# Kernel optimization log

Measured on AMD Instinct MI355X. Metric: run time of the kernel, lower is better.

Reference implementation:

```python
import jax, jax.numpy as jnp
import numpy as np

# model constants (match init_kwargs)
D_EQUI = 64
D_INV = 256
D_INV_COND = 256
D_MSG = 64
N_HEADS = 16
D_FF = 256
D_EDGE_IN = 64
D_EDGE_OUT = 64
D_OUT = D_EQUI + N_HEADS + D_EDGE_OUT  # 144
IN_FEATS = 2 * D_MSG + D_EQUI + D_EDGE_IN  # 256
NEG = -1e9

B, N, NC = 2, 256, 512


def setup_inputs() -> dict:
    key = jax.random.key(0)
    ks = jax.random.split(key, 20)
    s = 0.02
    inp = {
        'equis': jax.random.normal(ks[0], (B, N, 3, D_EQUI), jnp.float32),
        'invs': jax.random.normal(ks[1], (B, N, D_INV), jnp.float32),
        'cond_equis': jax.random.normal(ks[2], (B, NC, 3, D_EQUI), jnp.float32),
        'cond_invs': jax.random.normal(ks[3], (B, NC, D_INV_COND), jnp.float32),
        'edges': jax.random.normal(ks[4], (B, N, NC, D_EDGE_IN), jnp.float32),
        'adj_matrix': jax.random.randint(ks[5], (B, N, NC), 0, 2, jnp.int32),
        # pairwise message params
        'q_w': s * jax.random.normal(ks[6], (D_INV, D_MSG), jnp.float32),
        'q_b': jnp.zeros((D_MSG,), jnp.float32),
        'k_w': s * jax.random.normal(ks[7], (D_INV_COND, D_MSG), jnp.float32),
        'k_b': jnp.zeros((D_MSG,), jnp.float32),
        'w1': s * jax.random.normal(ks[8], (IN_FEATS, D_FF), jnp.float32),
        'b1': jnp.zeros((D_FF,), jnp.float32),
        'w2': s * jax.random.normal(ks[9], (D_FF, D_OUT), jnp.float32),
        'b2': jnp.zeros((D_OUT,), jnp.float32),
        # equi attention params (bias-free linears)
        'equi_in_w': s * jax.random.normal(ks[10], (D_EQUI, D_EQUI), jnp.float32),
        'equi_out_w': s * jax.random.normal(ks[11], (D_EQUI, D_EQUI), jnp.float32),
        # inv attention params
        'inv_in_w': s * jax.random.normal(ks[12], (D_INV_COND, D_INV_COND), jnp.float32),
        'inv_in_b': jnp.zeros((D_INV_COND,), jnp.float32),
        'inv_out_w': s * jax.random.normal(ks[13], (D_INV_COND, D_INV), jnp.float32),
        'inv_out_b': jnp.zeros((D_INV,), jnp.float32),
    }
    return inp


def reference(equis, invs, cond_equis, cond_invs, edges, adj_matrix,
              q_w, q_b, k_w, k_b, w1, b1, w2, b2,
              equi_in_w, equi_out_w, inv_in_w, inv_in_b, inv_out_w, inv_out_b):
    # adjacency -> additive attention mask [B,N,NC]
    mask = jnp.where(adj_matrix > 0, 0.0, NEG).astype(equis.dtype)

    # ---- pairwise messages ----
    # per-channel dot products over the coordinate axis: [B,N,NC,D_EQUI]
    dot = jnp.einsum('bqxd,bkxd->bqkd', equis, cond_equis)
    q_msg = invs @ q_w + q_b            # [B,N,D_MSG]
    k_msg = cond_invs @ k_w + k_b       # [B,NC,D_MSG]
    feats = jnp.concatenate([
        jnp.broadcast_to(q_msg[:, :, None, :], (B, N, NC, D_MSG)),
        jnp.broadcast_to(k_msg[:, None, :, :], (B, N, NC, D_MSG)),
        dot,
        edges,
    ], axis=-1)                          # [B,N,NC,IN_FEATS]
    h = jax.nn.silu(feats @ w1 + b1)
    messages = h @ w2 + b2               # [B,N,NC,D_OUT]

    equi_m = messages[..., :D_EQUI]
    inv_m = messages[..., D_EQUI:D_EQUI + N_HEADS]
    edge_out = messages[..., D_EQUI + N_HEADS:]

    # ---- equivariant attention ----
    proj = jnp.einsum('bkxd,de->bkxe', cond_equis, equi_in_w)  # [B,NC,3,D_EQUI]
    attn_e = jax.nn.softmax(equi_m + mask[..., None], axis=2)   # [B,N,NC,D_EQUI]
    eo = jnp.einsum('bqkd,bkxd->bqxd', attn_e, proj)            # [B,N,3,D_EQUI]
    w_e = jnp.sqrt(jnp.sum(attn_e ** 2, axis=2))                # [B,N,D_EQUI]
    eo = eo * w_e[:, :, None, :]
    equi_out = jnp.einsum('bqxd,de->bqxe', eo, equi_out_w)

    # ---- invariant attention ----
    pf = cond_invs @ inv_in_w + inv_in_b                        # [B,NC,D_INV_COND]
    hf = pf.reshape(B, NC, N_HEADS, D_INV_COND // N_HEADS)      # [B,NC,H,dh]
    attn_i = jax.nn.softmax(inv_m + mask[..., None], axis=2)    # [B,N,NC,H]
    io = jnp.einsum('bqkh,bkhd->bqhd', attn_i, hf)              # [B,N,H,dh]
    w_i = jnp.sqrt(jnp.sum(attn_i ** 2, axis=2))                # [B,N,H]
    io = (io * w_i[..., None]).reshape(B, N, D_INV_COND)
    inv_out = io @ inv_out_w + inv_out_b                        # [B,N,D_INV]

    return equi_out, inv_out, edge_out
```

## Files before the change

kernel.cpp:

```cpp
#include <hip/hip_runtime.h>
#include <hip/hip_bf16.h>

#define DEVINL static __device__ __forceinline__

typedef __attribute__((ext_vector_type(8))) short bf16x8;
typedef __attribute__((ext_vector_type(8))) unsigned short us8;
typedef __attribute__((ext_vector_type(4))) float f32x4;
typedef __attribute__((ext_vector_type(4))) unsigned short us4;

DEVINL float siluf(float x) { return x / (1.0f + __expf(-x)); }
DEVINL unsigned short bfb(float x) { __hip_bfloat16 h = __float2bfloat16(x); return *(unsigned short*)&h; }
DEVINL float b2f(unsigned short u) { return __uint_as_float(((unsigned int)u) << 16); }

__global__ void wfrag_kernel(const float* __restrict__ w1, const float* __restrict__ w2,
                             unsigned short* __restrict__ w1f, unsigned short* __restrict__ w2f) {
  const int g = blockIdx.x, tid = threadIdx.x;
  if (g < 16) {
    #pragma unroll
    for (int e2 = 0; e2 < 16; ++e2) {
      const int flat = tid * 16 + e2;
      const int kk = flat >> 9, rem = flat & 511, ln = rem >> 3, e = rem & 7;
      const int c = g * 16 + (ln & 15);
      const int k = kk * 32 + (ln >> 4) * 8 + e;
      w1f[(size_t)g * 4096 + flat] = bfb(w1[(size_t)k * 256 + c]);
    }
  } else {
    const int t = g - 16;
    #pragma unroll
    for (int e2 = 0; e2 < 16; ++e2) {
      const int flat = tid * 16 + e2;
      const int kk = flat >> 9, rem = flat & 511, ln = rem >> 3, e = rem & 7;
      const int c = t * 16 + (ln & 15);
      const int k = kk * 32 + (ln >> 4) * 8 + e;
      w2f[(size_t)t * 4096 + flat] = bfb(w2[(size_t)k * 144 + c]);
    }
  }
}

__global__ void qk_kernel(const float* __restrict__ invs, const float* __restrict__ cond_invs,
                          const float* __restrict__ qw, const float* __restrict__ qb,
                          const float* __restrict__ kw, const float* __restrict__ kb2,
                          float* __restrict__ qm, float* __restrict__ km) {
  __shared__ float srow[256];
  const int r = blockIdx.x;
  const float* in; const float* w; const float* bias; float* out; int row;
  if (r < 512) { in = invs;      w = qw; bias = qb;  out = qm; row = r; }
  else         { in = cond_invs; w = kw; bias = kb2; out = km; row = r - 512; }
  for (int k = threadIdx.x; k < 256; k += 64) srow[k] = in[(size_t)row * 256 + k];
  __syncthreads();
  const int c = threadIdx.x;
  float acc = bias[c];
  for (int k = 0; k < 256; ++k) acc += srow[k] * w[(size_t)k * 64 + c];
  out[(size_t)row * 64 + c] = acc;
}

__global__ void projt_kernel(const float* __restrict__ ce, const float* __restrict__ eiw,
                             float* __restrict__ projt) {
  __shared__ float srow[64];
  const int r = blockIdx.x;
  const int b = r / 1536, rr = r % 1536, kn = rr / 3, x = rr % 3;
  srow[threadIdx.x] = ce[(size_t)r * 64 + threadIdx.x];
  __syncthreads();
  const int c = threadIdx.x;
  float acc = 0.f;
  for (int k = 0; k < 64; ++k) acc += srow[k] * eiw[(size_t)k * 64 + c];
  projt[((size_t)(b * 3 + x) * 64 + c) * 512 + kn] = acc;
}

__global__ void pft_kernel(const float* __restrict__ ci, const float* __restrict__ iiw,
                           const float* __restrict__ iib, float* __restrict__ pft) {
  __shared__ float srow[256];
  const int r = blockIdx.x, b = r >> 9, kn = r & 511;
  srow[threadIdx.x] = ci[(size_t)r * 256 + threadIdx.x];
  __syncthreads();
  const int c = threadIdx.x;
  float acc = iib[c];
  for (int k = 0; k < 256; ++k) acc += srow[k] * iiw[(size_t)k * 256 + c];
  pft[((size_t)(b * 256) + c) * 512 + kn] = acc;
}

__global__ __launch_bounds__(256, 2) void msg_kernel(
    const float* __restrict__ equis, const float* __restrict__ cond_equis,
    const float* __restrict__ edges,
    const float* __restrict__ qm, const float* __restrict__ km,
    const unsigned short* __restrict__ w1f, const float* __restrict__ b1,
    const unsigned short* __restrict__ w2f, const float* __restrict__ b2,
    float* __restrict__ edge_out, __hip_bfloat16* __restrict__ sct) {
  __shared__ __align__(16) unsigned short buf[64][264];
  __shared__ float eq_s[192];
  unsigned short (*score_s)[92] = (unsigned short (*)[92])&buf[0][0];
  float (*edge_s)[68]           = (float (*)[68])((char*)&buf[0][0] + 11776);

  const int bq = blockIdx.x >> 3;
  const int b  = bq >> 8;
  const int k0 = (blockIdx.x & 7) * 64;
  const int tid = threadIdx.x;
  const int lane = tid & 63, wn = tid >> 6;
  const int lj  = lane & 15;
  const int lkb = (lane >> 4) * 8;
  const int lr4 = (lane >> 4) * 4;

  if (tid < 192) eq_s[tid] = equis[(size_t)bq * 192 + tid];

  bf16x8 qf[2];
  {
    const float* qmr = qm + (size_t)bq * 64;
    #pragma unroll
    for (int kk = 0; kk < 2; ++kk) {
      const float4 a = *(const float4*)&qmr[kk * 32 + (lane >> 4) * 8];
      const float4 c = *(const float4*)&qmr[kk * 32 + (lane >> 4) * 8 + 4];
      bf16x8 v;
      v[0] = (short)bfb(a.x); v[1] = (short)bfb(a.y); v[2] = (short)bfb(a.z); v[3] = (short)bfb(a.w);
      v[4] = (short)bfb(c.x); v[5] = (short)bfb(c.y); v[6] = (short)bfb(c.z); v[7] = (short)bfb(c.w);
      qf[kk] = v;
    }
  }
  __syncthreads();

  #pragma unroll
  for (int it = 0; it < 4; ++it) {
    const int flat = it * 256 + tid, row = flat >> 4, seg = flat & 15;
    const float4 v = *(const float4*)&km[((size_t)(b * 512 + k0 + row)) * 64 + seg * 4];
    us4 u = { bfb(v.x), bfb(v.y), bfb(v.z), bfb(v.w) };
    *(us4*)&buf[row][seg * 4] = u;
  }
  #pragma unroll
  for (int it = 0; it < 4; ++it) {
    const int flat = it * 256 + tid, row = flat >> 4, seg = flat & 15;
    const float4 v = *(const float4*)&edges[((size_t)bq * 512 + k0 + row) * 64 + seg * 4];
    us4 u = { bfb(v.x), bfb(v.y), bfb(v.z), bfb(v.w) };
    *(us4*)&buf[row][128 + seg * 4] = u;
  }
  {
    const int r = tid >> 2, dseg = tid & 3;
    const float* cer = cond_equis + ((size_t)(b * 512 + k0 + r)) * 192 + dseg * 16;
    float dv[16];
    #pragma unroll
    for (int j = 0; j < 16; ++j) dv[j] = 0.f;
    #pragma unroll
    for (int sec = 0; sec < 3; ++sec) {
      #pragma unroll
      for (int q4 = 0; q4 < 4; ++q4) {
        const float4 cv = *(const float4*)&cer[sec * 64 + q4 * 4];
        const float4 ev = *(const float4*)&eq_s[sec * 64 + dseg * 16 + q4 * 4];
        dv[q4 * 4 + 0] += cv.x * ev.x;
        dv[q4 * 4 + 1] += cv.y * ev.y;
        dv[q4 * 4 + 2] += cv.z * ev.z;
        dv[q4 * 4 + 3] += cv.w * ev.w;
      }
    }
    us8 o0, o1;
    #pragma unroll
    for (int j = 0; j < 8; ++j) { o0[j] = bfb(dv[j]); o1[j] = bfb(dv[8 + j]); }
    *(us8*)&buf[r][64 + dseg * 16] = o0;
    *(us8*)&buf[r][64 + dseg * 16 + 8] = o1;
  }
  __syncthreads();

#define LW1(BUF, KK) { \
    _Pragma("unroll") for (int ct = 0; ct < 4; ++ct) \
      BUF[ct] = *(const bf16x8*)&w1f[((size_t)(((wn * 4 + ct) * 8 + (KK)) * 64) + lane) * 8]; }

#define G1STEP(KK, CUR, NXT, DOPF) { \
    if (DOPF) { LW1(NXT, (KK) + 1); } \
    if ((KK) < 2) { \
      _Pragma("unroll") for (int ct = 0; ct < 4; ++ct) \
        _Pragma("unroll") for (int rt = 0; rt < 4; ++rt) \
          acc[ct][rt] = __builtin_amdgcn_mfma_f32_16x16x32_bf16(CUR[ct], qf[KK], acc[ct][rt], 0, 0, 0); \
    } else { \
      bf16x8 fbv[4]; \
      _Pragma("unroll") for (int rt = 0; rt < 4; ++rt) \
        fbv[rt] = *(const bf16x8*)&buf[rt * 16 + lj][((KK) - 2) * 32 + lkb]; \
      _Pragma("unroll") for (int ct = 0; ct < 4; ++ct) \
        _Pragma("unroll") for (int rt = 0; rt < 4; ++rt) \
          acc[ct][rt] = __builtin_amdgcn_mfma_f32_16x16x32_bf16(CUR[ct], fbv[rt], acc[ct][rt], 0, 0, 0); \
    } }

#define LW2(BUF, KK) { \
    _Pragma("unroll") for (int it = 0; it < 3; ++it) { \
      const int t = it * 4 + wn; \
      if (t < 9) BUF[it] = *(const bf16x8*)&w2f[((size_t)((t * 8 + (KK)) * 64) + lane) * 8]; } }

#define G2STEP(KK, CUR, NXT, DOPF) { \
    if (DOPF) { LW2(NXT, (KK) + 1); } \
    bf16x8 fbv[4]; \
    _Pragma("unroll") for (int rt = 0; rt < 4; ++rt) \
      fbv[rt] = *(const bf16x8*)&buf[rt * 16 + lj][(KK) * 32 + lkb]; \
    _Pragma("unroll") for (int it = 0; it < 3; ++it) { \
      const int t = it * 4 + wn; \
      if (t < 9) { \
        _Pragma("unroll") for (int rt = 0; rt < 4; ++rt) \
          a2[it][rt] = __builtin_amdgcn_mfma_f32_16x16x32_bf16(CUR[it], fbv[rt], a2[it][rt], 0, 0, 0); \
      } } }

  f32x4 acc[4][4];
  #pragma unroll
  for (int ct = 0; ct < 4; ++ct) {
    const float4 bb = *(const float4*)&b1[wn * 64 + ct * 16 + lr4];
    #pragma unroll
    for (int rt = 0; rt < 4; ++rt) { acc[ct][rt][0] = bb.x; acc[ct][rt][1] = bb.y; acc[ct][rt][2] = bb.z; acc[ct][rt][3] = bb.w; }
  }
  {
    bf16x8 waA[4], waB[4];
    LW1(waA, 0);
    G1STEP(0, waA, waB, 1)
    G1STEP(1, waB, waA, 1)
    G1STEP(2, waA, waB, 1)
    G1STEP(3, waB, waA, 1)
    G1STEP(4, waA, waB, 1)
    G1STEP(5, waB, waA, 1)
    G1STEP(6, waA, waB, 1)
    G1STEP(7, waB, waA, 0)
  }
  __syncthreads();

  #pragma unroll
  for (int ct = 0; ct < 4; ++ct)
    #pragma unroll
    for (int rt = 0; rt < 4; ++rt) {
      us4 u = { bfb(siluf(acc[ct][rt][0])), bfb(siluf(acc[ct][rt][1])),
                bfb(siluf(acc[ct][rt][2])), bfb(siluf(acc[ct][rt][3])) };
      *(us4*)&buf[rt * 16 + lj][wn * 64 + ct * 16 + lr4] = u;
    }
  __syncthreads();

  f32x4 a2[3][4];
  #pragma unroll
  for (int it = 0; it < 3; ++it) {
    const int t = it * 4 + wn;
    if (t < 9) {
      const float4 bb = *(const float4*)&b2[t * 16 + lr4];
      #pragma unroll
      for (int rt = 0; rt < 4; ++rt) { a2[it][rt][0] = bb.x; a2[it][rt][1] = bb.y; a2[it][rt][2] = bb.z; a2[it][rt][3] = bb.w; }
    }
  }
  {
    bf16x8 wbA[3], wbB[3];
    LW2(wbA, 0);
    G2STEP(0, wbA, wbB, 1)
    G2STEP(1, wbB, wbA, 1)
    G2STEP(2, wbA, wbB, 1)
    G2STEP(3, wbB, wbA, 1)
    G2STEP(4, wbA, wbB, 1)
    G2STEP(5, wbB, wbA, 1)
    G2STEP(6, wbA, wbB, 1)
    G2STEP(7, wbB, wbA, 0)
  }
  __syncthreads();

  #pragma unroll
  for (int it = 0; it < 3; ++it) {
    const int t = it * 4 + wn;
    if (t < 9) {
      if (t < 5) {
        #pragma unroll
        for (int rt = 0; rt < 4; ++rt) {
          us4 u = { bfb(a2[it][rt][0]), bfb(a2[it][rt][1]), bfb(a2[it][rt][2]), bfb(a2[it][rt][3]) };
          *(us4*)&score_s[rt * 16 + lj][t * 16 + lr4] = u;
        }
      } else {
        #pragma unroll
        for (int rt = 0; rt < 4; ++rt) {
          float4 v; v.x = a2[it][rt][0]; v.y = a2[it][rt][1]; v.z = a2[it][rt][2]; v.w = a2[it][rt][3];
          *(float4*)&edge_s[rt * 16 + lj][(t - 5) * 16 + lr4] = v;
        }
      }
    }
  }
  __syncthreads();

  #pragma unroll
  for (int it = 0; it < 3; ++it) {
    const int idx = it * 256 + tid;
    if (idx < 640) {
      const int c = idx >> 3, s = idx & 7;
      bf16x8 v;
      #pragma unroll
      for (int j = 0; j < 8; ++j) v[j] = (short)score_s[s * 8 + j][c];
      *(bf16x8*)&sct[((size_t)bq * 80 + c) * 512 + k0 + s * 8] = v;
    }
  }
  #pragma unroll
  for (int it = 0; it < 4; ++it) {
    const int idx = it * 256 + tid;
    const int row = idx >> 4, sg = idx & 15;
    *(float4*)&edge_out[((size_t)bq * 512 + k0 + row) * 64 + sg * 4] = *(const float4*)&edge_s[row][sg * 4];
  }
#undef LW1
#undef G1STEP
#undef LW2
#undef G2STEP
}

__global__ __launch_bounds__(512) void attn_kernel(
    const __hip_bfloat16* __restrict__ sct, const int* __restrict__ adj,
    const float* __restrict__ projt, const float* __restrict__ pft,
    const float* __restrict__ eow, const float* __restrict__ iow,
    const float* __restrict__ iob, float* __restrict__ out) {
  __shared__ float eo_s[3][64];
  __shared__ float io_s[256];

  const int bq = blockIdx.x, b = bq >> 8;
  const int tid = threadIdx.x, lane = tid & 63, w = tid >> 6;
  const int kb = lane * 8;

  const int4 aj0 = *(const int4*)&adj[(size_t)bq * 512 + kb];
  const int4 aj1 = *(const int4*)&adj[(size_t)bq * 512 + kb + 4];
  const unsigned int mk = (aj0.x > 0 ? 1u : 0) | (aj0.y > 0 ? 2u : 0) | (aj0.z > 0 ? 4u : 0) | (aj0.w > 0 ? 8u : 0)
                        | (aj1.x > 0 ? 16u : 0) | (aj1.y > 0 ? 32u : 0) | (aj1.z > 0 ? 64u : 0) | (aj1.w > 0 ? 128u : 0);

  for (int dd = 0; dd < 8; ++dd) {
    const int d = w * 8 + dd;
    const bf16x8 s8 = *(const bf16x8*)&sct[((size_t)bq * 80 + d) * 512 + kb];
    float p[8], z = 0.f, s2 = 0.f;
    #pragma unroll
    for (int j = 0; j < 8; ++j) {
      const float e = ((mk >> j) & 1) ? __expf(b2f((unsigned short)s8[j])) : 0.f;
      p[j] = e; z += e; s2 += e * e;
    }
    float ax[3];
    #pragma unroll
    for (int x = 0; x < 3; ++x) {
      const float* pr = projt + ((size_t)(b * 3 + x) * 64 + d) * 512 + kb;
      const float4 w0 = *(const float4*)pr;
      const float4 w1v = *(const float4*)(pr + 4);
      ax[x] = p[0] * w0.x + p[1] * w0.y + p[2] * w0.z + p[3] * w0.w
            + p[4] * w1v.x + p[5] * w1v.y + p[6] * w1v.z + p[7] * w1v.w;
    }
    #pragma unroll
    for (int off = 32; off; off >>= 1) {
      z += __shfl_xor(z, off, 64); s2 += __shfl_xor(s2, off, 64);
      ax[0] += __shfl_xor(ax[0], off, 64); ax[1] += __shfl_xor(ax[1], off, 64); ax[2] += __shfl_xor(ax[2], off, 64);
    }
    if (lane == 0) {
      const float sc = sqrtf(s2) / (z * z);
      eo_s[0][d] = ax[0] * sc; eo_s[1][d] = ax[1] * sc; eo_s[2][d] = ax[2] * sc;
    }
  }

  #pragma unroll
  for (int hh = 0; hh < 2; ++hh) {
    const int h = w * 2 + hh;
    const bf16x8 s8 = *(const bf16x8*)&sct[((size_t)bq * 80 + 64 + h) * 512 + kb];
    float p[8], z = 0.f, s2 = 0.f;
    #pragma unroll
    for (int j = 0; j < 8; ++j) {
      const float e = ((mk >> j) & 1) ? __expf(b2f((unsigned short)s8[j])) : 0.f;
      p[j] = e; z += e; s2 += e * e;
    }
    f32x4 io[4];
    #pragma unroll
    for (int d4 = 0; d4 < 4; ++d4)
      #pragma unroll
      for (int di = 0; di < 4; ++di) {
        const float* pr = pft + ((size_t)(b * 256) + h * 16 + d4 * 4 + di) * 512 + kb;
        const float4 w0 = *(const float4*)pr;
        const float4 w1v = *(const float4*)(pr + 4);
        io[d4][di] = p[0] * w0.x + p[1] * w0.y + p[2] * w0.z + p[3] * w0.w
                   + p[4] * w1v.x + p[5] * w1v.y + p[6] * w1v.z + p[7] * w1v.w;
      }
    #pragma unroll
    for (int off = 32; off; off >>= 1) {
      z += __shfl_xor(z, off, 64); s2 += __shfl_xor(s2, off, 64);
      #pragma unroll
      for (int d4 = 0; d4 < 4; ++d4)
        #pragma unroll
        for (int di = 0; di < 4; ++di)
          io[d4][di] += __shfl_xor(io[d4][di], off, 64);
    }
    if (lane == 0) {
      const float sc = sqrtf(s2) / (z * z);
      #pragma unroll
      for (int d4 = 0; d4 < 4; ++d4) {
        float4 vv; vv.x = io[d4][0] * sc; vv.y = io[d4][1] * sc; vv.z = io[d4][2] * sc; vv.w = io[d4][3] * sc;
        *(float4*)&io_s[h * 16 + d4 * 4] = vv;
      }
    }
  }
  __syncthreads();

  if (tid < 192) {
    const int x = tid >> 6, e = tid & 63;
    float a = 0.f;
    for (int d = 0; d < 64; ++d) a += eo_s[x][d] * eow[(size_t)d * 64 + e];
    out[(size_t)bq * 192 + x * 64 + e] = a;
  }
  if (tid < 256) {
    float a = iob[tid];
    for (int k = 0; k < 256; ++k) a += io_s[k] * iow[(size_t)k * 256 + tid];
    out[98304 + (size_t)bq * 256 + tid] = a;
  }
}

extern "C" void kernel_launch(void* const* d_in, const int* in_sizes, int n_in,
                              void* d_out, int out_size, void* d_ws, size_t ws_size,
                              hipStream_t stream) {
  const float* equis      = (const float*)d_in[0];
  const float* invs       = (const float*)d_in[1];
  const float* cond_equis = (const float*)d_in[2];
  const float* cond_invs  = (const float*)d_in[3];
  const float* edges      = (const float*)d_in[4];
  const int*   adj        = (const int*)d_in[5];
  const float* q_w  = (const float*)d_in[6];
  const float* q_b  = (const float*)d_in[7];
  const float* k_w  = (const float*)d_in[8];
  const float* k_b  = (const float*)d_in[9];
  const float* w1   = (const float*)d_in[10];
  const float* b1   = (const float*)d_in[11];
  const float* w2   = (const float*)d_in[12];
  const float* b2   = (const float*)d_in[13];
  const float* equi_in_w  = (const float*)d_in[14];
  const float* equi_out_w = (const float*)d_in[15];
  const float* inv_in_w   = (const float*)d_in[16];
  const float* inv_in_b   = (const float*)d_in[17];
  const float* inv_out_w  = (const float*)d_in[18];
  const float* inv_out_b  = (const float*)d_in[19];

  float* out = (float*)d_out;
  float* ws  = (float*)d_ws;
  unsigned short* w1f = (unsigned short*)ws;
  unsigned short* w2f = w1f + 65536;
  float* qm    = ws + 51200;
  float* km    = qm + 32768;
  float* projt = km + 65536;
  float* pft   = projt + 196608;
  __hip_bfloat16* sct = (__hip_bfloat16*)(pft + 262144);

  wfrag_kernel<<<25, 256, 0, stream>>>(w1, w2, w1f, w2f);
  qk_kernel<<<1536, 64, 0, stream>>>(invs, cond_invs, q_w, q_b, k_w, k_b, qm, km);
  projt_kernel<<<3072, 64, 0, stream>>>(cond_equis, equi_in_w, projt);
  pft_kernel<<<1024, 256, 0, stream>>>(cond_invs, inv_in_w, inv_in_b, pft);

  msg_kernel<<<4096, 256, 0, stream>>>(equis, cond_equis, edges, qm, km,
                                       w1f, b1, w2f, b2,
                                       out + 229376 , sct);

  attn_kernel<<<512, 512, 0, stream>>>(sct, adj, projt, pft,
                                       equi_out_w, inv_out_w, inv_out_b, out);
}
```

Measured before the change: 167.2 us.

## Fold query projection into hoisted per-row hidden bias and merge prep kernels

The query message is constant across all key positions of a row, so its contribution through the first FFN layer (q·W1[0:64] + b1) is precomputed once per query row in a new prep stage and used to initialise the accumulators. This removes two of eight K-steps of MFMA work in the message kernel. The four small preprocessing kernels are merged into one launch. The attention kernel's cross-lane reduction of the per-head output now goes through LDS instead of 16 shuffle chains. The hidden-bias precompute stays in fp32, which changes rounding slightly versus the bf16 MFMA path. The LDS reduction adds about 40KB of shared memory per attention block, which may reduce occupancy.

```diff
diff --git a/kernel.cpp b/kernel.cpp
--- a/kernel.cpp
+++ b/kernel.cpp
@@ -12,82 +12,99 @@
 DEVINL unsigned short bfb(float x) { __hip_bfloat16 h = __float2bfloat16(x); return *(unsigned short*)&h; }
 DEVINL float b2f(unsigned short u) { return __uint_as_float(((unsigned int)u) << 16); }
 
-__global__ void wfrag_kernel(const float* __restrict__ w1, const float* __restrict__ w2,
-                             unsigned short* __restrict__ w1f, unsigned short* __restrict__ w2f) {
-  const int g = blockIdx.x, tid = threadIdx.x;
-  if (g < 16) {
-    #pragma unroll
-    for (int e2 = 0; e2 < 16; ++e2) {
-      const int flat = tid * 16 + e2;
-      const int kk = flat >> 9, rem = flat & 511, ln = rem >> 3, e = rem & 7;
-      const int c = g * 16 + (ln & 15);
-      const int k = kk * 32 + (ln >> 4) * 8 + e;
-      w1f[(size_t)g * 4096 + flat] = bfb(w1[(size_t)k * 256 + c]);
-    }
-  } else {
-    const int t = g - 16;
-    #pragma unroll
-    for (int e2 = 0; e2 < 16; ++e2) {
-      const int flat = tid * 16 + e2;
-      const int kk = flat >> 9, rem = flat & 511, ln = rem >> 3, e = rem & 7;
-      const int c = t * 16 + (ln & 15);
-      const int k = kk * 32 + (ln >> 4) * 8 + e;
-      w2f[(size_t)t * 4096 + flat] = bfb(w2[(size_t)k * 144 + c]);
-    }
-  }
-}
-
-__global__ void qk_kernel(const float* __restrict__ invs, const float* __restrict__ cond_invs,
-                          const float* __restrict__ qw, const float* __restrict__ qb,
-                          const float* __restrict__ kw, const float* __restrict__ kb2,
-                          float* __restrict__ qm, float* __restrict__ km) {
-  __shared__ float srow[256];
-  const int r = blockIdx.x;
-  const float* in; const float* w; const float* bias; float* out; int row;
-  if (r < 512) { in = invs;      w = qw; bias = qb;  out = qm; row = r; }
-  else         { in = cond_invs; w = kw; bias = kb2; out = km; row = r - 512; }
-  for (int k = threadIdx.x; k < 256; k += 64) srow[k] = in[(size_t)row * 256 + k];
-  __syncthreads();
-  const int c = threadIdx.x;
-  float acc = bias[c];
-  for (int k = 0; k < 256; ++k) acc += srow[k] * w[(size_t)k * 64 + c];
-  out[(size_t)row * 64 + c] = acc;
-}
-
-__global__ void projt_kernel(const float* __restrict__ ce, const float* __restrict__ eiw,
-                             float* __restrict__ projt) {
-  __shared__ float srow[64];
-  const int r = blockIdx.x;
-  const int b = r / 1536, rr = r % 1536, kn = rr / 3, x = rr % 3;
-  srow[threadIdx.x] = ce[(size_t)r * 64 + threadIdx.x];
-  __syncthreads();
-  const int c = threadIdx.x;
-  float acc = 0.f;
-  for (int k = 0; k < 64; ++k) acc += srow[k] * eiw[(size_t)k * 64 + c];
-  projt[((size_t)(b * 3 + x) * 64 + c) * 512 + kn] = acc;
-}
-
-__global__ void pft_kernel(const float* __restrict__ ci, const float* __restrict__ iiw,
-                           const float* __restrict__ iib, float* __restrict__ pft) {
-  __shared__ float srow[256];
-  const int r = blockIdx.x, b = r >> 9, kn = r & 511;
-  srow[threadIdx.x] = ci[(size_t)r * 256 + threadIdx.x];
-  __syncthreads();
-  const int c = threadIdx.x;
-  float acc = iib[c];
-  for (int k = 0; k < 256; ++k) acc += srow[k] * iiw[(size_t)k * 256 + c];
-  pft[((size_t)(b * 256) + c) * 512 + kn] = acc;
+__global__ __launch_bounds__(256) void prep_all(
+    const float* __restrict__ invs, const float* __restrict__ cond_invs,
+    const float* __restrict__ cond_equis,
+    const float* __restrict__ q_w, const float* __restrict__ q_b,
+    const float* __restrict__ k_w, const float* __restrict__ k_b,
+    const float* __restrict__ w1, const float* __restrict__ b1,
+    const float* __restrict__ w2,
+    const float* __restrict__ equi_in_w,
+    const float* __restrict__ inv_in_w, const float* __restrict__ inv_in_b,
+    unsigned short* __restrict__ w1f, unsigned short* __restrict__ w2f,
+    float* __restrict__ km, float* __restrict__ hq,
+    float* __restrict__ projt, float* __restrict__ pft) {
+  __shared__ float smem_f[1024];
+  const int blk = blockIdx.x, tid = threadIdx.x;
+
+  if (blk < 25) {
+    const int g = blk;
+    if (g < 16) {
+      #pragma unroll
+      for (int e2 = 0; e2 < 16; ++e2) {
+        const int flat = tid * 16 + e2;
+        const int kk = flat >> 9, rem = flat & 511, ln = rem >> 3, e = rem & 7;
+        const int c = g * 16 + (ln & 15);
+        const int k = kk * 32 + (ln >> 4) * 8 + e;
+        w1f[(size_t)g * 4096 + flat] = bfb(w1[(size_t)k * 256 + c]);
+      }
+    } else {
+      const int t = g - 16;
+      #pragma unroll
+      for (int e2 = 0; e2 < 16; ++e2) {
+        const int flat = tid * 16 + e2;
+        const int kk = flat >> 9, rem = flat & 511, ln = rem >> 3, e = rem & 7;
+        const int c = t * 16 + (ln & 15);
+        const int k = kk * 32 + (ln >> 4) * 8 + e;
+        w2f[(size_t)t * 4096 + flat] = bfb(w2[(size_t)k * 144 + c]);
+      }
+    }
+    return;
+  }
+  if (blk < 281) {
+    const int row = (blk - 25) * 4 + (tid >> 6), c = tid & 63;
+    float* srow = smem_f + (tid >> 6) * 256;
+    for (int k = c; k < 256; k += 64) srow[k] = cond_invs[(size_t)row * 256 + k];
+    __syncthreads();
+    float a = k_b[c];
+    for (int k = 0; k < 256; ++k) a += srow[k] * k_w[(size_t)k * 64 + c];
+    km[(size_t)row * 64 + c] = a;
+    return;
+  }
+  if (blk < 1049) {
+    const int r = (blk - 281) * 4 + (tid >> 6), c = tid & 63;
+    float* srow = smem_f + (tid >> 6) * 64;
+    srow[c] = cond_equis[(size_t)r * 64 + c];
+    __syncthreads();
+    float a = 0.f;
+    for (int k = 0; k < 64; ++k) a += srow[k] * equi_in_w[(size_t)k * 64 + c];
+    const int b = r / 1536, rr = r % 1536, kn = rr / 3, x = rr % 3;
+    projt[((size_t)(b * 3 + x) * 64 + c) * 512 + kn] = a;
+    return;
+  }
+  if (blk < 2073) {
+    const int r = blk - 1049, b = r >> 9, kn = r & 511;
+    smem_f[tid] = cond_invs[(size_t)r * 256 + tid];
+    __syncthreads();
+    float a = inv_in_b[tid];
+    for (int k = 0; k < 256; ++k) a += smem_f[k] * inv_in_w[(size_t)k * 256 + tid];
+    pft[((size_t)(b * 256) + tid) * 512 + kn] = a;
+    return;
+  }
+  {
+    const int r = blk - 2073;
+    smem_f[tid] = invs[(size_t)r * 256 + tid];
+    __syncthreads();
+    if (tid < 64) {
+      float a = q_b[tid];
+      for (int k = 0; k < 256; ++k) a += smem_f[k] * q_w[(size_t)k * 64 + tid];
+      smem_f[256 + tid] = a;
+    }
+    __syncthreads();
+    float a = b1[tid];
+    for (int d = 0; d < 64; ++d) a += smem_f[256 + d] * w1[(size_t)d * 256 + tid];
+    hq[(size_t)r * 256 + tid] = a;
+  }
 }
 
 __global__ __launch_bounds__(256, 2) void msg_kernel(
     const float* __restrict__ equis, const float* __restrict__ cond_equis,
     const float* __restrict__ edges,
-    const float* __restrict__ qm, const float* __restrict__ km,
-    const unsigned short* __restrict__ w1f, const float* __restrict__ b1,
+    const float* __restrict__ hq, const float* __restrict__ km,
+    const unsigned short* __restrict__ w1f,
     const unsigned short* __restrict__ w2f, const float* __restrict__ b2,
     float* __restrict__ edge_out, __hip_bfloat16* __restrict__ sct) {
   __shared__ __align__(16) unsigned short buf[64][264];
-  __shared__ float eq_s[192];
   unsigned short (*score_s)[92] = (unsigned short (*)[92])&buf[0][0];
   float (*edge_s)[68]           = (float (*)[68])((char*)&buf[0][0] + 11776);
 
@@ -100,23 +117,6 @@
   const int lkb = (lane >> 4) * 8;
   const int lr4 = (lane >> 4) * 4;
 
-  if (tid < 192) eq_s[tid] = equis[(size_t)bq * 192 + tid];
-
-  bf16x8 qf[2];
-  {
-    const float* qmr = qm + (size_t)bq * 64;
-    #pragma unroll
-    for (int kk = 0; kk < 2; ++kk) {
-      const float4 a = *(const float4*)&qmr[kk * 32 + (lane >> 4) * 8];
-      const float4 c = *(const float4*)&qmr[kk * 32 + (lane >> 4) * 8 + 4];
-      bf16x8 v;
-      v[0] = (short)bfb(a.x); v[1] = (short)bfb(a.y); v[2] = (short)bfb(a.z); v[3] = (short)bfb(a.w);
-      v[4] = (short)bfb(c.x); v[5] = (short)bfb(c.y); v[6] = (short)bfb(c.z); v[7] = (short)bfb(c.w);
-      qf[kk] = v;
-    }
-  }
-  __syncthreads();
-
   #pragma unroll
   for (int it = 0; it < 4; ++it) {
     const int flat = it * 256 + tid, row = flat >> 4, seg = flat & 15;
@@ -134,6 +134,7 @@
   {
     const int r = tid >> 2, dseg = tid & 3;
     const float* cer = cond_equis + ((size_t)(b * 512 + k0 + r)) * 192 + dseg * 16;
+    const float* eqr = equis + (size_t)bq * 192 + dseg * 16;
     float dv[16];
     #pragma unroll
     for (int j = 0; j < 16; ++j) dv[j] = 0.f;
@@ -142,7 +143,7 @@
       #pragma unroll
       for (int q4 = 0; q4 < 4; ++q4) {
         const float4 cv = *(const float4*)&cer[sec * 64 + q4 * 4];
-        const float4 ev = *(const float4*)&eq_s[sec * 64 + dseg * 16 + q4 * 4];
+        const float4 ev = *(const float4*)&eqr[sec * 64 + q4 * 4];
         dv[q4 * 4 + 0] += cv.x * ev.x;
         dv[q4 * 4 + 1] += cv.y * ev.y;
         dv[q4 * 4 + 2] += cv.z * ev.z;
@@ -159,22 +160,16 @@
 
 #define LW1(BUF, KK) { \
     _Pragma("unroll") for (int ct = 0; ct < 4; ++ct) \
-      BUF[ct] = *(const bf16x8*)&w1f[((size_t)(((wn * 4 + ct) * 8 + (KK)) * 64) + lane) * 8]; }
+      BUF[ct] = *(const bf16x8*)&w1f[((size_t)(((wn * 4 + ct) * 8 + ((KK) + 2)) * 64) + lane) * 8]; }
 
 #define G1STEP(KK, CUR, NXT, DOPF) { \
     if (DOPF) { LW1(NXT, (KK) + 1); } \
-    if ((KK) < 2) { \
-      _Pragma("unroll") for (int ct = 0; ct < 4; ++ct) \
-        _Pragma("unroll") for (int rt = 0; rt < 4; ++rt) \
-          acc[ct][rt] = __builtin_amdgcn_mfma_f32_16x16x32_bf16(CUR[ct], qf[KK], acc[ct][rt], 0, 0, 0); \
-    } else { \
-      bf16x8 fbv[4]; \
+    bf16x8 fbv[4]; \
+    _Pragma("unroll") for (int rt = 0; rt < 4; ++rt) \
+      fbv[rt] = *(const bf16x8*)&buf[rt * 16 + lj][(KK) * 32 + lkb]; \
+    _Pragma("unroll") for (int ct = 0; ct < 4; ++ct) \
       _Pragma("unroll") for (int rt = 0; rt < 4; ++rt) \
-        fbv[rt] = *(const bf16x8*)&buf[rt * 16 + lj][((KK) - 2) * 32 + lkb]; \
-      _Pragma("unroll") for (int ct = 0; ct < 4; ++ct) \
-        _Pragma("unroll") for (int rt = 0; rt < 4; ++rt) \
-          acc[ct][rt] = __builtin_amdgcn_mfma_f32_16x16x32_bf16(CUR[ct], fbv[rt], acc[ct][rt], 0, 0, 0); \
-    } }
+        acc[ct][rt] = __builtin_amdgcn_mfma_f32_16x16x32_bf16(CUR[ct], fbv[rt], acc[ct][rt], 0, 0, 0); }
 
 #define LW2(BUF, KK) { \
     _Pragma("unroll") for (int it = 0; it < 3; ++it) { \
@@ -196,9 +191,9 @@
   f32x4 acc[4][4];
   #pragma unroll
   for (int ct = 0; ct < 4; ++ct) {
-    const float4 bb = *(const float4*)&b1[wn * 64 + ct * 16 + lr4];
-    #pragma unroll
-    for (int rt = 0; rt < 4; ++rt) { acc[ct][rt][0] = bb.x; acc[ct][rt][1] = bb.y; acc[ct][rt][2] = bb.z; acc[ct][rt][3] = bb.w; }
+    const float4 hv = *(const float4*)&hq[(size_t)bq * 256 + wn * 64 + ct * 16 + lr4];
+    #pragma unroll
+    for (int rt = 0; rt < 4; ++rt) { acc[ct][rt][0] = hv.x; acc[ct][rt][1] = hv.y; acc[ct][rt][2] = hv.z; acc[ct][rt][3] = hv.w; }
   }
   {
     bf16x8 waA[4], waB[4];
@@ -208,9 +203,7 @@
     G1STEP(2, waA, waB, 1)
     G1STEP(3, waB, waA, 1)
     G1STEP(4, waA, waB, 1)
-    G1STEP(5, waB, waA, 1)
-    G1STEP(6, waA, waB, 1)
-    G1STEP(7, waB, waA, 0)
+    G1STEP(5, waB, waA, 0)
   }
   __syncthreads();
 
@@ -299,6 +292,7 @@
     const float* __restrict__ iob, float* __restrict__ out) {
   __shared__ float eo_s[3][64];
   __shared__ float io_s[256];
+  __shared__ __align__(16) float wred[8][64][20];
 
   const int bq = blockIdx.x, b = bq >> 8;
   const int tid = threadIdx.x, lane = tid & 63, w = tid >> 6;
@@ -360,21 +354,21 @@
                    + p[4] * w1v.x + p[5] * w1v.y + p[6] * w1v.z + p[7] * w1v.w;
       }
     #pragma unroll
-    for (int off = 32; off; off >>= 1) {
-      z += __shfl_xor(z, off, 64); s2 += __shfl_xor(s2, off, 64);
-      #pragma unroll
-      for (int d4 = 0; d4 < 4; ++d4)
-        #pragma unroll
-        for (int di = 0; di < 4; ++di)
-          io[d4][di] += __shfl_xor(io[d4][di], off, 64);
-    }
-    if (lane == 0) {
+    for (int off = 32; off; off >>= 1) { z += __shfl_xor(z, off, 64); s2 += __shfl_xor(s2, off, 64); }
+    #pragma unroll
+    for (int d4 = 0; d4 < 4; ++d4) {
+      float4 vv; vv.x = io[d4][0]; vv.y = io[d4][1]; vv.z = io[d4][2]; vv.w = io[d4][3];
+      *(float4*)&wred[w][lane][d4 * 4] = vv;
+    }
+    const int g = lane >> 4, dd2 = lane & 15;
+    float s = 0.f;
+    #pragma unroll
+    for (int j = 0; j < 16; ++j) s += wred[w][g * 16 + j][dd2];
+    s += __shfl_xor(s, 16, 64);
+    s += __shfl_xor(s, 32, 64);
+    if (lane < 16) {
       const float sc = sqrtf(s2) / (z * z);
-      #pragma unroll
-      for (int d4 = 0; d4 < 4; ++d4) {
-        float4 vv; vv.x = io[d4][0] * sc; vv.y = io[d4][1] * sc; vv.z = io[d4][2] * sc; vv.w = io[d4][3] * sc;
-        *(float4*)&io_s[h * 16 + d4 * 4] = vv;
-      }
+      io_s[h * 16 + dd2] = s * sc;
     }
   }
   __syncthreads();
@@ -420,19 +414,19 @@
   float* ws  = (float*)d_ws;
   unsigned short* w1f = (unsigned short*)ws;
   unsigned short* w2f = w1f + 65536;
-  float* qm    = ws + 51200;
-  float* km    = qm + 32768;
-  float* projt = km + 65536;
+  float* km    = ws + 51200;
+  float* hq    = km + 65536;
+  float* projt = hq + 131072;
   float* pft   = projt + 196608;
   __hip_bfloat16* sct = (__hip_bfloat16*)(pft + 262144);
 
-  wfrag_kernel<<<25, 256, 0, stream>>>(w1, w2, w1f, w2f);
-  qk_kernel<<<1536, 64, 0, stream>>>(invs, cond_invs, q_w, q_b, k_w, k_b, qm, km);
-  projt_kernel<<<3072, 64, 0, stream>>>(cond_equis, equi_in_w, projt);
-  pft_kernel<<<1024, 256, 0, stream>>>(cond_invs, inv_in_w, inv_in_b, pft);
-
-  msg_kernel<<<4096, 256, 0, stream>>>(equis, cond_equis, edges, qm, km,
-                                       w1f, b1, w2f, b2,
+  prep_all<<<2585, 256, 0, stream>>>(invs, cond_invs, cond_equis,
+                                     q_w, q_b, k_w, k_b, w1, b1, w2,
+                                     equi_in_w, inv_in_w, inv_in_b,
+                                     w1f, w2f, km, hq, projt, pft);
+
+  msg_kernel<<<4096, 256, 0, stream>>>(equis, cond_equis, edges, hq, km,
+                                       w1f, w2f, b2,
                                        out + 229376 , sct);
 
   attn_kernel<<<512, 512, 0, stream>>>(sct, adj, projt, pft,
```

Result: faster. 156.5 us (-6.4%).
